# Kernel tuning notes

Hardware: AMD Instinct MI355X
Metric: run time of the kernel (lower is better)

The kernel has to match this reference:

```python
import jax, jax.numpy as jnp
import numpy as np

B, L, H, W, C = 2, 16, 64, 64, 256


def _pconv(x5, Wm, b):
    # 1x1x1 Conv3d == pointwise channel linear. x5: (B,C,L,H,W), Wm: (Cout,Cin), b: (Cout,)
    return jnp.einsum('bclhw,oc->bolhw', x5, Wm) + b[None, :, None, None, None]


def setup_inputs() -> dict:
    key = jax.random.key(0)
    ks = jax.random.split(key, 9)
    s = 0.02  # small init so softmax logits (sum over HW=4096) stay in a sane range
    x = jax.random.normal(ks[0], (B, L, H, W, C), jnp.float32)
    prev_features = jax.random.normal(ks[1], (B, L, H, W, C), jnp.float32)
    Wq = jax.random.normal(ks[2], (C, C), jnp.float32) * s
    bq = jax.random.normal(ks[3], (C,), jnp.float32) * s
    Wk = jax.random.normal(ks[4], (C, C), jnp.float32) * s
    bk = jax.random.normal(ks[5], (C,), jnp.float32) * s
    Wv = jax.random.normal(ks[6], (C, C), jnp.float32) * s
    bv = jax.random.normal(ks[7], (C,), jnp.float32) * s
    gamma = jnp.array([0.5], jnp.float32)  # torch init is 0; use 0.5 so the attention path is exercised
    return {'x': x, 'prev_features': prev_features, 'Wq': Wq, 'bq': bq,
            'Wk': Wk, 'bk': bk, 'Wv': Wv, 'bv': bv, 'gamma': gamma}


def reference(x, prev_features, Wq, bq, Wk, bk, Wv, bv, gamma):
    # x, prev_features: (B, L, H, W, C) channel-last
    x5 = jnp.transpose(x, (0, 4, 1, 2, 3))              # (B,C,L,H,W)
    p5 = jnp.transpose(prev_features, (0, 4, 1, 2, 3))  # (B,C,L,H,W)
    b_, c_, l_, h_, w_ = x5.shape
    n = b_ * l_
    hw = h_ * w_
    # Q: (B,C,L,H,W)->(B,L,C,H,W)->(BL, C, HW)
    q = jnp.transpose(_pconv(x5, Wq, bq), (0, 2, 1, 3, 4)).reshape(n, c_, hw)
    # K: (B,C,L,H,W)->(B,L,C,W,H)->(BL, C, HW)  (note W,H swap before flatten, as in torch)
    k = jnp.transpose(_pconv(p5, Wk, bk), (0, 2, 1, 4, 3)).reshape(n, c_, hw)
    # attention[n,c,d] = sum_s q[n,c,s] * k[n,d,s]  -> (BL, C, C), softmax over d
    attn = jax.nn.softmax(jnp.einsum('ncs,nds->ncd', q, k), axis=-1)
    # V: raw contiguous reshape of (B,C,L,H,W) into (BL, C, HW) -- faithful to torch's buggy reshape
    v = _pconv(p5, Wv, bv).reshape(n, c_, hw)
    # out[n,s,c] = sum_d v[n,d,s] * attn[n,c,d]   (== bmm(v^T, attn^T))
    out = jnp.einsum('nds,ncd->nsc', v, attn).reshape(b_, l_, h_, w_, c_)
    # x5.permute(0,2,3,4,1) recovers the original x
    return gamma * out + x
```

## Files before the change

kernel.cpp:

```cpp
#include <hip/hip_runtime.h>
#include <hip/hip_bf16.h>


typedef short short8 __attribute__((ext_vector_type(8)));
typedef short short4v __attribute__((ext_vector_type(4)));
typedef float f32x4 __attribute__((ext_vector_type(4)));

static __device__ __forceinline__ unsigned short f2bf(float f) {
  union { __hip_bfloat16 h; unsigned short u; } cv;
  cv.h = __float2bfloat16(f);
  return cv.u;
}

__global__ __launch_bounds__(256) void k_convert_w(const float* __restrict__ wq,
                                                   const float* __restrict__ wk,
                                                   const float* __restrict__ wv,
                                                   unsigned short* __restrict__ o) {
  int i = blockIdx.x * 256 + threadIdx.x;
  const float* s = (i < 65536) ? wq : (i < 131072 ? wk : wv);
  o[i] = f2bf(s[i & 65535]);
}

template <int MODE>
__global__ __launch_bounds__(256) void k_qkv(const float* __restrict__ src,
                                             const unsigned short* __restrict__ w,
                                             const float* __restrict__ bias,
                                             unsigned short* __restrict__ dst) {
  __shared__ __align__(16) unsigned short inp[64 * 264];
  __shared__ __align__(16) unsigned short wc[256 * 72];
  const int t = threadIdx.x;
  int n, wcol, s0;
  if (MODE == 1) {
    n = blockIdx.x >> 6; wcol = blockIdx.x & 63; s0 = 0;
  } else {
    n = blockIdx.x >> 6; wcol = 0; s0 = (blockIdx.x & 63) << 6;
  }
#pragma unroll
  for (int i = 0; i < 16; ++i) {
    int q = i * 256 + t;
    int row = q >> 6;
    int c4 = (q & 63) << 2;
    size_t srow = (MODE == 1) ? (size_t)(n * 4096 + row * 64 + wcol)
                              : (size_t)(n * 4096 + s0 + row);
    float4 v = *(const float4*)(src + srow * 256 + c4);
    unsigned short* p = &inp[row * 264 + c4];
    p[0] = f2bf(v.x); p[1] = f2bf(v.y); p[2] = f2bf(v.z); p[3] = f2bf(v.w);
  }
  const int wid = t >> 6, lane = t & 63;
  const int l16 = lane & 15, lk = (lane >> 4) << 3;
  f32x4 acc[16];
#pragma unroll
  for (int i = 0; i < 16; ++i) acc[i] = (f32x4){0.f, 0.f, 0.f, 0.f};
  const unsigned short* arow = &inp[(wid * 16 + l16) * 264];
  const int wo = t >> 3, wch = t & 7;
  for (int kc = 0; kc < 4; ++kc) {
    __syncthreads();
#pragma unroll
    for (int p = 0; p < 8; ++p) {
      const int o = p * 32 + wo;
      short8 wv = *(const short8*)(w + o * 256 + kc * 64 + wch * 8);
      *(short8*)&wc[o * 72 + wch * 8] = wv;
    }
    __syncthreads();
#pragma unroll
    for (int ks2 = 0; ks2 < 64; ks2 += 32) {
      short8 a = *(const short8*)(arow + kc * 64 + ks2 + lk);
#pragma unroll
      for (int nt = 0; nt < 16; ++nt) {
        short8 b = *(const short8*)(&wc[(nt * 16 + l16) * 72 + ks2 + lk]);
        acc[nt] = __builtin_amdgcn_mfma_f32_16x16x32_bf16(a, b, acc[nt], 0, 0, 0);
      }
    }
  }
  __syncthreads();
  const int sl0 = wid * 16 + ((lane >> 4) << 2);
#pragma unroll
  for (int nt = 0; nt < 16; ++nt) {
    const int o = nt * 16 + l16;
    const float bo = bias[o];
    short4v pk;
#pragma unroll
    for (int j = 0; j < 4; ++j) pk[j] = (short)f2bf(acc[nt][j] + bo);
    *(short4v*)&wc[o * 72 + sl0] = pk;
  }
  __syncthreads();
  const int co = t >> 3, ch = t & 7;
#pragma unroll
  for (int p = 0; p < 8; ++p) {
    const int o = p * 32 + co;
    short8 v = *(const short8*)&wc[o * 72 + ch * 8];
    size_t base;
    if (MODE == 0) {
      base = ((size_t)n << 20) + (size_t)o * 4096 + (size_t)(s0 + ch * 8);
    } else if (MODE == 1) {
      base = ((size_t)n << 20) + (size_t)o * 4096 + (size_t)(wcol * 64 + ch * 8);
    } else {
      const int b_ = n >> 4, l_ = n & 15;
      base = (size_t)((b_ * 256 + o) * 16 + l_) * 4096 + (size_t)(s0 + ch * 8);
    }
    *(short8*)(dst + base) = v;
  }
}

__global__ __launch_bounds__(256) void k_vt(const unsigned short* __restrict__ vb,
                                            unsigned short* __restrict__ vt) {
  __shared__ unsigned short lds[64 * 264];
  const int t = threadIdx.x;
  const int np = blockIdx.x >> 6;
  const int s0 = (blockIdx.x & 63) << 6;
  const int b = np >> 4, chi = np & 15;
  const int d0 = (t & 127) << 1, sh = (t >> 7) << 5;
  const int c = chi * 16 + (d0 >> 4);
  const int l0 = d0 & 15;
  const unsigned short* r0p = vb + (size_t)((b * 256 + c) * 16 + l0) * 4096 + s0 + sh;
  const unsigned short* r1p = r0p + 4096;
#pragma unroll
  for (int i = 0; i < 4; ++i) {
    short8 a = *(const short8*)(r0p + i * 8);
    short8 bb = *(const short8*)(r1p + i * 8);
#pragma unroll
    for (int j = 0; j < 8; ++j) {
      int s = sh + i * 8 + j;
      unsigned int pk = (unsigned int)(unsigned short)a[j] |
                        ((unsigned int)(unsigned short)bb[j] << 16);
      *(unsigned int*)&lds[s * 264 + d0] = pk;
    }
  }
  __syncthreads();
  const int sl = t >> 2, ch = t & 3;
  unsigned short* outp = vt + ((size_t)np << 20) + (size_t)(s0 + sl) * 256 + ch * 64;
  const unsigned short* lp = &lds[sl * 264 + ch * 64];
#pragma unroll
  for (int i = 0; i < 8; ++i)
    *(short8*)(outp + i * 8) = *(const short8*)(lp + i * 8);
}

__global__ __launch_bounds__(256) void k_logits(const unsigned short* __restrict__ qb,
                                                const unsigned short* __restrict__ kb,
                                                float* __restrict__ attn) {
  __shared__ __align__(16) unsigned short qt[2][64 * 64];
  __shared__ __align__(16) unsigned short kt[2][128 * 64];
  const int n = blockIdx.z;
  const int kh = blockIdx.y;
  const int c0 = (blockIdx.x >> 1) * 64;
  const int d0 = (blockIdx.x & 1) * 128;
  const int t = threadIdx.x, wid = t >> 6, lane = t & 63;
  const int l16 = lane & 15, l4 = lane >> 4;
  const int wr = wid >> 1, wc = wid & 1;
  const int koff0 = kh * 2048;
  const unsigned short* qg = qb + ((size_t)n << 20) + (size_t)c0 * 4096 + koff0;
  const unsigned short* kg = kb + ((size_t)n << 20) + (size_t)d0 * 4096 + koff0;
  const int srow8 = wid * 8 + (lane >> 3);
  const int schunk = lane & 7;

  int arow[2], brow[4];
#pragma unroll
  for (int mt = 0; mt < 2; ++mt) arow[mt] = wr * 32 + mt * 16 + l16;
#pragma unroll
  for (int nt = 0; nt < 4; ++nt) brow[nt] = wc * 64 + nt * 16 + l16;

  f32x4 acc[2][4];
#pragma unroll
  for (int mt = 0; mt < 2; ++mt)
#pragma unroll
    for (int nt = 0; nt < 4; ++nt) acc[mt][nt] = (f32x4){0.f, 0.f, 0.f, 0.f};

#define STAGE(buf, kc)                                                          \
  {                                                                             \
    const int ko = (kc) * 64;                                                   \
    _Pragma("unroll")                                                           \
    for (int i = 0; i < 2; ++i) {                                               \
      const int row = i * 32 + srow8;                                           \
      const int cg = schunk ^ (row & 7);                                        \
      const unsigned short* g = qg + (size_t)row * 4096 + ko + cg * 8;          \
      unsigned short* l = &qt[buf][i * 2048 + wid * 512];                       \
      __builtin_amdgcn_global_load_lds(                                         \
          (const __attribute__((address_space(1))) unsigned int*)(const void*)g,\
          (__attribute__((address_space(3))) unsigned int*)(void*)l, 16, 0, 0); \
    }                                                                           \
    _Pragma("unroll")                                                           \
    for (int i = 0; i < 4; ++i) {                                               \
      const int row = i * 32 + srow8;                                           \
      const int cg = schunk ^ (row & 7);                                        \
      const unsigned short* g = kg + (size_t)row * 4096 + ko + cg * 8;          \
      unsigned short* l = &kt[buf][i * 2048 + wid * 512];                       \
      __builtin_amdgcn_global_load_lds(                                         \
          (const __attribute__((address_space(1))) unsigned int*)(const void*)g,\
          (__attribute__((address_space(3))) unsigned int*)(void*)l, 16, 0, 0); \
    }                                                                           \
  }

  int cur = 0;
  STAGE(0, 0);
  __syncthreads();
  for (int kc = 0; kc < 32; ++kc) {
    if (kc < 31) STAGE(cur ^ 1, kc + 1);
    short8 bf[4][2];
#pragma unroll
    for (int nt = 0; nt < 4; ++nt)
#pragma unroll
      for (int ks = 0; ks < 2; ++ks)
        bf[nt][ks] = *(const short8*)&kt[cur][brow[nt] * 64 +
                                             (((ks * 4 + l4) ^ (brow[nt] & 7)) << 3)];
#pragma unroll
    for (int mt = 0; mt < 2; ++mt) {
      short8 a0 = *(const short8*)&qt[cur][arow[mt] * 64 + ((l4 ^ (arow[mt] & 7)) << 3)];
      short8 a1 = *(const short8*)&qt[cur][arow[mt] * 64 + (((4 + l4) ^ (arow[mt] & 7)) << 3)];
#pragma unroll
      for (int nt = 0; nt < 4; ++nt) {
        acc[mt][nt] = __builtin_amdgcn_mfma_f32_16x16x32_bf16(a0, bf[nt][0], acc[mt][nt], 0, 0, 0);
        acc[mt][nt] = __builtin_amdgcn_mfma_f32_16x16x32_bf16(a1, bf[nt][1], acc[mt][nt], 0, 0, 0);
      }
    }
    __syncthreads();
    cur ^= 1;
  }
#undef STAGE
  float* ah = attn + (size_t)kh * 2097152 + (size_t)n * 65536;
#pragma unroll
  for (int mt = 0; mt < 2; ++mt)
#pragma unroll
    for (int nt = 0; nt < 4; ++nt) {
      const int d = d0 + wc * 64 + nt * 16 + l16;
#pragma unroll
      for (int j = 0; j < 4; ++j) {
        const int c = c0 + wr * 32 + mt * 16 + (l4 << 2) + j;
        ah[(size_t)c * 256 + d] = acc[mt][nt][j];
      }
    }
}

__global__ __launch_bounds__(256) void k_softmax(const float* __restrict__ attn,
                                                 unsigned short* __restrict__ abf) {
  const int t = threadIdx.x, wid = t >> 6, lane = t & 63;
  const int row = blockIdx.x * 4 + wid;
  const int n = row >> 8, c = row & 255;
  const float* p0 = attn + (size_t)n * 65536 + (size_t)c * 256;
  const float* p1 = p0 + 2097152;
  float v0 = p0[lane] + p1[lane];
  float v1 = p0[lane + 64] + p1[lane + 64];
  float v2 = p0[lane + 128] + p1[lane + 128];
  float v3 = p0[lane + 192] + p1[lane + 192];
  float m = fmaxf(fmaxf(v0, v1), fmaxf(v2, v3));
#pragma unroll
  for (int off = 32; off >= 1; off >>= 1) m = fmaxf(m, __shfl_xor(m, off, 64));
  float e0 = __expf(v0 - m), e1 = __expf(v1 - m), e2 = __expf(v2 - m), e3 = __expf(v3 - m);
  float s = e0 + e1 + e2 + e3;
#pragma unroll
  for (int off = 32; off >= 1; off >>= 1) s += __shfl_xor(s, off, 64);
  const float inv = 1.0f / s;
  unsigned short* q = abf + (size_t)n * 65536 + (size_t)c * 256;
  q[lane]       = f2bf(e0 * inv);
  q[lane + 64]  = f2bf(e1 * inv);
  q[lane + 128] = f2bf(e2 * inv);
  q[lane + 192] = f2bf(e3 * inv);
}

__global__ __launch_bounds__(256) void k_out(const unsigned short* __restrict__ vT,
                                             const unsigned short* __restrict__ abf,
                                             const float* __restrict__ x,
                                             const float* __restrict__ gamma,
                                             float* __restrict__ out) {
  __shared__ __align__(16) unsigned short bsm[64 * 264];
  const int n = blockIdx.z;
  const int c0 = blockIdx.y * 64;
  const int s0 = blockIdx.x * 64;
  const int t = threadIdx.x, wid = t >> 6, lane = t & 63;
  const int l16 = lane & 15, lk = (lane >> 4) << 3;
  {
    const int rr = t >> 5, ch = t & 31;
#pragma unroll
    for (int i = 0; i < 8; ++i) {
      const int row = rr + i * 8;
      short8 v = *(const short8*)(abf + (size_t)n * 65536 + (size_t)(c0 + row) * 256 + ch * 8);
      *(short8*)&bsm[row * 264 + ch * 8] = v;
    }
  }
  __syncthreads();
  const unsigned short* arow = vT + (size_t)n * 1048576 + (size_t)(s0 + wid * 16 + l16) * 256 + lk;
  f32x4 acc[4];
#pragma unroll
  for (int i = 0; i < 4; ++i) acc[i] = (f32x4){0.f, 0.f, 0.f, 0.f};
#pragma unroll
  for (int ks = 0; ks < 256; ks += 32) {
    short8 a = *(const short8*)(arow + ks);
#pragma unroll
    for (int nt = 0; nt < 4; ++nt) {
      short8 b = *(const short8*)(&bsm[(nt * 16 + l16) * 264 + ks + lk]);
      acc[nt] = __builtin_amdgcn_mfma_f32_16x16x32_bf16(a, b, acc[nt], 0, 0, 0);
    }
  }
  __syncthreads();
  float* ldsf = (float*)bsm;
  const int sl0 = wid * 16 + ((lane >> 4) << 2);
#pragma unroll
  for (int nt = 0; nt < 4; ++nt)
#pragma unroll
    for (int j = 0; j < 4; ++j)
      ldsf[(sl0 + j) * 68 + nt * 16 + l16] = acc[nt][j];
  __syncthreads();
  const float g = gamma[0];
  const int ch = t & 15, rr = t >> 4;
#pragma unroll
  for (int i = 0; i < 4; ++i) {
    const int row = rr + i * 16;
    f32x4 v = *(const f32x4*)&ldsf[row * 68 + ch * 4];
    const size_t addr = ((size_t)n * 4096 + (size_t)(s0 + row)) * 256 + (size_t)(c0 + ch * 4);
    float4 xv = *(const float4*)(x + addr);
    float4 ov;
    ov.x = g * v[0] + xv.x; ov.y = g * v[1] + xv.y;
    ov.z = g * v[2] + xv.z; ov.w = g * v[3] + xv.w;
    *(float4*)(out + addr) = ov;
  }
}

extern "C" void kernel_launch(void* const* d_in, const int* in_sizes, int n_in,
                              void* d_out, int out_size, void* d_ws, size_t ws_size,
                              hipStream_t stream) {
  const float* x    = (const float*)d_in[0];
  const float* prev = (const float*)d_in[1];
  const float* Wq   = (const float*)d_in[2];
  const float* bq   = (const float*)d_in[3];
  const float* Wk   = (const float*)d_in[4];
  const float* bk   = (const float*)d_in[5];
  const float* Wv   = (const float*)d_in[6];
  const float* bv   = (const float*)d_in[7];
  const float* gamma = (const float*)d_in[8];

  char* ws = (char*)d_ws;
  unsigned short* qv   = (unsigned short*)ws;
  unsigned short* kbuf = (unsigned short*)(ws + 67108864ULL);
  float* attn          = (float*)(ws + 134217728ULL);
  unsigned short* abf  = (unsigned short*)(ws + 150994944ULL);
  unsigned short* wbf  = (unsigned short*)(ws + 155189248ULL);

  k_convert_w<<<dim3(768), dim3(256), 0, stream>>>(Wq, Wk, Wv, wbf);
  k_qkv<0><<<dim3(2048), dim3(256), 0, stream>>>(x, wbf, bq, qv);
  k_qkv<1><<<dim3(2048), dim3(256), 0, stream>>>(prev, wbf + 65536, bk, kbuf);
  k_logits<<<dim3(8, 2, 32), dim3(256), 0, stream>>>(qv, kbuf, attn);
  k_qkv<2><<<dim3(2048), dim3(256), 0, stream>>>(prev, wbf + 131072, bv, kbuf);
  k_softmax<<<dim3(2048), dim3(256), 0, stream>>>(attn, abf);
  k_vt<<<dim3(2048), dim3(256), 0, stream>>>(kbuf, qv);
  k_out<<<dim3(64, 4, 32), dim3(256), 0, stream>>>(qv, abf, x, gamma, (float*)d_out);
}
```

Measured before the change: 574.3 us.

## Restructure QKV projection GEMM with 4x4 MFMA tiles, swizzled LDS and async weight loads

The QKV projection kernel now streams the input in 64-channel chunks instead of staging the whole 64x256 input tile, which shrinks LDS use and allows four blocks per CU via launch bounds. Each wave computes a 4x4 grid of MFMA tiles, reusing A and B fragments across tiles, instead of a 1x16 strip that reloaded B for every tile. The weight matrix is pre-swizzled during the bf16 conversion so it can be copied straight into LDS with global_load_lds, and an XOR swizzle replaces row padding to avoid bank conflicts. The trade-off is more complex index arithmetic and one barrier per k-chunk that must cover the asynchronous LDS loads.

```diff
diff --git a/kernel.cpp b/kernel.cpp
--- a/kernel.cpp
+++ b/kernel.cpp
@@ -15,19 +15,23 @@
 __global__ __launch_bounds__(256) void k_convert_w(const float* __restrict__ wq,
                                                    const float* __restrict__ wk,
                                                    const float* __restrict__ wv,
-                                                   unsigned short* __restrict__ o) {
+                                                   unsigned short* __restrict__ o2) {
   int i = blockIdx.x * 256 + threadIdx.x;
-  const float* s = (i < 65536) ? wq : (i < 131072 ? wk : wv);
-  o[i] = f2bf(s[i & 65535]);
+  int m = i >> 16;
+  const float* s = (m == 0) ? wq : (m == 1 ? wk : wv);
+  int r = i & 65535;
+  int kc = r >> 14, o = (r >> 6) & 255, pc = (r >> 3) & 7, j = r & 7;
+  int lc = pc ^ (o & 7);
+  o2[i] = f2bf(s[o * 256 + kc * 64 + lc * 8 + j]);
 }
 
 template <int MODE>
-__global__ __launch_bounds__(256) void k_qkv(const float* __restrict__ src,
-                                             const unsigned short* __restrict__ w,
-                                             const float* __restrict__ bias,
-                                             unsigned short* __restrict__ dst) {
-  __shared__ __align__(16) unsigned short inp[64 * 264];
-  __shared__ __align__(16) unsigned short wc[256 * 72];
+__global__ __launch_bounds__(256, 4) void k_qkv(const float* __restrict__ src,
+                                                const unsigned short* __restrict__ w,
+                                                const float* __restrict__ bias,
+                                                unsigned short* __restrict__ dst) {
+  __shared__ __align__(16) unsigned short inp[64 * 64];
+  __shared__ __align__(16) unsigned short wc[256 * 64];
   const int t = threadIdx.x;
   int n, wcol, s0;
   if (MODE == 1) {
@@ -35,60 +39,90 @@
   } else {
     n = blockIdx.x >> 6; wcol = 0; s0 = (blockIdx.x & 63) << 6;
   }
-#pragma unroll
-  for (int i = 0; i < 16; ++i) {
-    int q = i * 256 + t;
-    int row = q >> 6;
-    int c4 = (q & 63) << 2;
-    size_t srow = (MODE == 1) ? (size_t)(n * 4096 + row * 64 + wcol)
-                              : (size_t)(n * 4096 + s0 + row);
-    float4 v = *(const float4*)(src + srow * 256 + c4);
-    unsigned short* p = &inp[row * 264 + c4];
-    p[0] = f2bf(v.x); p[1] = f2bf(v.y); p[2] = f2bf(v.z); p[3] = f2bf(v.w);
-  }
   const int wid = t >> 6, lane = t & 63;
-  const int l16 = lane & 15, lk = (lane >> 4) << 3;
-  f32x4 acc[16];
-#pragma unroll
-  for (int i = 0; i < 16; ++i) acc[i] = (f32x4){0.f, 0.f, 0.f, 0.f};
-  const unsigned short* arow = &inp[(wid * 16 + l16) * 264];
-  const int wo = t >> 3, wch = t & 7;
+  const int l16 = lane & 15, lg = lane >> 4;
+  const int irow = t >> 2, iqc = t & 3;
+  const size_t isrow = (MODE == 1) ? (size_t)(n * 4096 + irow * 64 + wcol)
+                                   : (size_t)(n * 4096 + s0 + irow);
+  const float* isrc = src + isrow * 256 + iqc * 16;
+  const unsigned short* wsrc = w + (size_t)t * 8;
+
+  float bo[4];
+#pragma unroll
+  for (int nt = 0; nt < 4; ++nt) bo[nt] = bias[wid * 64 + nt * 16 + l16];
+
+  f32x4 acc[4][4];
+#pragma unroll
+  for (int mt = 0; mt < 4; ++mt)
+#pragma unroll
+    for (int nt = 0; nt < 4; ++nt) acc[mt][nt] = (f32x4){0.f, 0.f, 0.f, 0.f};
+
   for (int kc = 0; kc < 4; ++kc) {
+    if (kc) __syncthreads();
+#pragma unroll
+    for (int i = 0; i < 8; ++i) {
+      const unsigned short* g = wsrc + kc * 16384 + i * 2048;
+      unsigned short* l = &wc[i * 2048 + t * 8];
+      __builtin_amdgcn_global_load_lds(
+          (const __attribute__((address_space(1))) unsigned int*)(const void*)g,
+          (__attribute__((address_space(3))) unsigned int*)(void*)l, 16, 0, 0);
+    }
+    {
+      const float* p = isrc + kc * 64;
+      float4 v0 = *(const float4*)(p + 0),  v1 = *(const float4*)(p + 4);
+      float4 v2 = *(const float4*)(p + 8),  v3 = *(const float4*)(p + 12);
+      short8 c0, c1;
+      c0[0] = (short)f2bf(v0.x); c0[1] = (short)f2bf(v0.y);
+      c0[2] = (short)f2bf(v0.z); c0[3] = (short)f2bf(v0.w);
+      c0[4] = (short)f2bf(v1.x); c0[5] = (short)f2bf(v1.y);
+      c0[6] = (short)f2bf(v1.z); c0[7] = (short)f2bf(v1.w);
+      c1[0] = (short)f2bf(v2.x); c1[1] = (short)f2bf(v2.y);
+      c1[2] = (short)f2bf(v2.z); c1[3] = (short)f2bf(v2.w);
+      c1[4] = (short)f2bf(v3.x); c1[5] = (short)f2bf(v3.y);
+      c1[6] = (short)f2bf(v3.z); c1[7] = (short)f2bf(v3.w);
+      const int rx = irow & 7;
+      *(short8*)&inp[irow * 64 + (((iqc * 2) ^ rx) << 3)] = c0;
+      *(short8*)&inp[irow * 64 + (((iqc * 2 + 1) ^ rx) << 3)] = c1;
+    }
     __syncthreads();
 #pragma unroll
-    for (int p = 0; p < 8; ++p) {
-      const int o = p * 32 + wo;
-      short8 wv = *(const short8*)(w + o * 256 + kc * 64 + wch * 8);
-      *(short8*)&wc[o * 72 + wch * 8] = wv;
-    }
-    __syncthreads();
-#pragma unroll
-    for (int ks2 = 0; ks2 < 64; ks2 += 32) {
-      short8 a = *(const short8*)(arow + kc * 64 + ks2 + lk);
-#pragma unroll
-      for (int nt = 0; nt < 16; ++nt) {
-        short8 b = *(const short8*)(&wc[(nt * 16 + l16) * 72 + ks2 + lk]);
-        acc[nt] = __builtin_amdgcn_mfma_f32_16x16x32_bf16(a, b, acc[nt], 0, 0, 0);
-      }
-    }
-  }
-  __syncthreads();
-  const int sl0 = wid * 16 + ((lane >> 4) << 2);
-#pragma unroll
-  for (int nt = 0; nt < 16; ++nt) {
-    const int o = nt * 16 + l16;
-    const float bo = bias[o];
-    short4v pk;
-#pragma unroll
-    for (int j = 0; j < 4; ++j) pk[j] = (short)f2bf(acc[nt][j] + bo);
-    *(short4v*)&wc[o * 72 + sl0] = pk;
+    for (int ks2 = 0; ks2 < 2; ++ks2) {
+      const int lc = ks2 * 4 + lg;
+      const int px = (lc ^ (l16 & 7)) << 3;
+      short8 af[4], bf[4];
+#pragma unroll
+      for (int mt = 0; mt < 4; ++mt)
+        af[mt] = *(const short8*)&inp[(mt * 16 + l16) * 64 + px];
+#pragma unroll
+      for (int nt = 0; nt < 4; ++nt)
+        bf[nt] = *(const short8*)&wc[(wid * 64 + nt * 16 + l16) * 64 + px];
+#pragma unroll
+      for (int mt = 0; mt < 4; ++mt)
+#pragma unroll
+        for (int nt = 0; nt < 4; ++nt)
+          acc[mt][nt] = __builtin_amdgcn_mfma_f32_16x16x32_bf16(af[mt], bf[nt], acc[mt][nt], 0, 0, 0);
+    }
+  }
+  __syncthreads();
+#pragma unroll
+  for (int mt = 0; mt < 4; ++mt) {
+    const int sc = mt * 2 + (lg >> 1);
+    const int so = (lg & 1) * 4;
+#pragma unroll
+    for (int nt = 0; nt < 4; ++nt) {
+      const int o = wid * 64 + nt * 16 + l16;
+      short4v pk;
+#pragma unroll
+      for (int j = 0; j < 4; ++j) pk[j] = (short)f2bf(acc[mt][nt][j] + bo[nt]);
+      *(short4v*)&wc[o * 64 + ((sc ^ (o & 7)) << 3) + so] = pk;
+    }
   }
   __syncthreads();
   const int co = t >> 3, ch = t & 7;
 #pragma unroll
   for (int p = 0; p < 8; ++p) {
     const int o = p * 32 + co;
-    short8 v = *(const short8*)&wc[o * 72 + ch * 8];
+    short8 v = *(const short8*)&wc[o * 64 + ((ch ^ (o & 7)) << 3)];
     size_t base;
     if (MODE == 0) {
       base = ((size_t)n << 20) + (size_t)o * 4096 + (size_t)(s0 + ch * 8);
```

New measurement: 546.8 us. -4.8%, faster.
